# Performance work log

Measured on AMD Instinct MI355X. Metric: run time of the kernel, lower is better.

The kernel has to match this reference:

```python
import jax, jax.numpy as jnp
import numpy as np

THR = 0.2          # config['thr']
BORDER_RM = 2      # config['border_rm']
TEMP = 0.1         # config['dsmax_temperature']


def setup_inputs() -> dict:
    key = jax.random.key(0)
    k0, k1 = jax.random.split(key)
    N, C = 2, 256
    h0c, w0c, h1c, w1c = 60, 80, 60, 80
    return {
        "feat_c0": jax.random.normal(k0, (N, h0c * w0c, C), dtype=jnp.float32),
        "feat_c1": jax.random.normal(k1, (N, h1c * w1c, C), dtype=jnp.float32),
        "h0c": h0c, "w0c": w0c, "h1c": h1c, "w1c": w1c,
    }


def _valid_1d(n: int, b: int):
    # True in the interior [b, n-b), False on the border — matches mask_border writes
    return jnp.zeros((n,), dtype=bool).at[b:n - b].set(True)


def reference(feat_c0, feat_c1, h0c, w0c, h1c, w1c):
    N, L, C = feat_c0.shape
    S = feat_c1.shape[1]
    scale = 1.0 / (C ** 0.5)
    f0 = feat_c0 * scale
    f1 = feat_c1 * scale

    # similarity + dual softmax  -> conf_matrix [N, L, S]
    sim = jnp.einsum('nlc,nsc->nls', f0, f1) / TEMP
    conf = jax.nn.softmax(sim, axis=1) * jax.nn.softmax(sim, axis=2)

    # threshold + border removal (mask_border, vectorized as an interior mask)
    mask = conf > THR
    b = BORDER_RM
    border = (_valid_1d(h0c, b)[:, None, None, None]
              & _valid_1d(w0c, b)[None, :, None, None]
              & _valid_1d(h1c, b)[None, None, :, None]
              & _valid_1d(w1c, b)[None, None, None, :])  # [h0c,w0c,h1c,w1c]
    mask = (mask.reshape(N, h0c, w0c, h1c, w1c) & border[None]).reshape(N, L, S)

    # mutual nearest neighbor
    mask = mask \
        & (conf == conf.max(axis=2, keepdims=True)) \
        & (conf == conf.max(axis=1, keepdims=True))

    # match extraction, expressed densely (static shapes for jit):
    # mask_v[b,i] = row i of pair b has a match; j_ids its column; mconf its confidence
    mask_v = mask.any(axis=2)                               # [N, L]
    j_ids = jnp.argmax(mask, axis=2)                        # [N, L] (first True)
    mconf = jnp.take_along_axis(conf, j_ids[:, :, None], axis=2)[..., 0]
    mconf = jnp.where(mask_v, mconf, 0.0)                   # [N, L]

    # coarse keypoint coords for matched columns: (x, y) = (j % w1c, j // w1c)
    mkpts1_c = jnp.stack([j_ids % w1c, j_ids // w1c], axis=-1)  # [N, L, 2]

    return conf, mask_v, j_ids, mkpts1_c, mconf
```

## Files before the change

### kernel.cpp

```cpp
#include <hip/hip_runtime.h>

typedef _Float16 half8 __attribute__((ext_vector_type(8)));
typedef float f32x4 __attribute__((ext_vector_type(4)));

#define NB 2
#define LS 4800
#define CCH 256
#define W0 80
#define W1 80
#define THRV 0.2f
#define SQS 0.19764235376052370f

#define TN 38
#define PADL 4864

#define OF_RM   0
#define OF_RSI  9600
#define OF_CM   19200
#define OF_CSI  28800
#define OF_RWM  38400
#define OF_CAND 48000
#define OF_CLM  57600
#define OF_PROW 67200
#define OF_PCOL (67200 + 739328)
#define OF_AH   (67200 + 2*739328)
#define OF_BH   (OF_AH + 1228800)

#define O_MASKV 46080000ull
#define O_JIDS  46089600ull
#define O_MKPT  46099200ull
#define O_MCONF 46118400ull

__device__ __forceinline__ void load_lds16(const void* g, void* l) {
    __builtin_amdgcn_global_load_lds((const __attribute__((address_space(1))) void*)g,
                                     (__attribute__((address_space(3))) void*)l, 16, 0, 0);
}

__global__ __launch_bounds__(256) void conv_half(const float* __restrict__ A,
                                                 const float* __restrict__ B,
                                                 float* __restrict__ ws) {
    const int which = blockIdx.y;
    const float* src = which ? B : A;
    _Float16* dst = (_Float16*)(ws + (which ? OF_BH : OF_AH));
    const int idx = blockIdx.x * 256 + threadIdx.x;
    const float4 v = ((const float4*)src)[idx];
    union { _Float16 h[4]; uint2 u; } p;
    p.h[0] = (_Float16)(v.x * SQS);
    p.h[1] = (_Float16)(v.y * SQS);
    p.h[2] = (_Float16)(v.z * SQS);
    p.h[3] = (_Float16)(v.w * SQS);
    ((uint2*)dst)[idx] = p.u;
}

__global__ __launch_bounds__(256, 2) void gemm_mfma(float* __restrict__ out,
                                                    float* __restrict__ ws) {
    __shared__ __align__(16) union {
        struct { _Float16 A[8192]; _Float16 B[8192]; } st;
        struct { float rs[128][2][2]; float cs[128][2][2]; } red;
    } sm;
    const int bx = blockIdx.x, by = blockIdx.y, n = blockIdx.z;
    const _Float16* Ah = (const _Float16*)(ws + OF_AH) + (size_t)n * LS * CCH;
    const _Float16* Bh = (const _Float16*)(ws + OF_BH) + (size_t)n * LS * CCH;
    const int tid = threadIdx.x;
    const int lane = tid & 63, w = tid >> 6;
    const int wx = w & 1, wy = w >> 1;
    const int m = lane & 15, quad = lane >> 4;

    f32x4 acc[4][4];
    {
        f32x4 z = {0.f, 0.f, 0.f, 0.f};
#pragma unroll
        for (int a = 0; a < 4; a++)
#pragma unroll
            for (int b = 0; b < 4; b++) acc[a][b] = z;
    }

    const int srow = lane >> 3;
    const int qst = (lane & 7) ^ (srow & 7);

    for (int kt = 0; kt < 4; kt++) {
        const int k0 = kt * 64;
#pragma unroll
        for (int i = 0; i < 4; i++) {
            const int c = i * 4 + w;
            int gr = by * 128 + c * 8 + srow; gr = gr < LS ? gr : LS - 1;
            load_lds16(Ah + (size_t)gr * CCH + k0 + qst * 8, &sm.st.A[c * 512]);
        }
#pragma unroll
        for (int i = 0; i < 4; i++) {
            const int c = i * 4 + w;
            int gr = bx * 128 + c * 8 + srow; gr = gr < LS ? gr : LS - 1;
            load_lds16(Bh + (size_t)gr * CCH + k0 + qst * 8, &sm.st.B[c * 512]);
        }
        __syncthreads();
#pragma unroll
        for (int t = 0; t < 2; t++) {
            half8 Af[4], Bf[4];
#pragma unroll
            for (int a = 0; a < 4; a++) {
                const int rl = wy * 64 + a * 16 + m;
                const int sl = rl * 8 + ((t * 4 + quad) ^ (rl & 7));
                Af[a] = *(const half8*)&sm.st.A[sl * 8];
            }
#pragma unroll
            for (int b = 0; b < 4; b++) {
                const int cl = wx * 64 + b * 16 + m;
                const int sl = cl * 8 + ((t * 4 + quad) ^ (cl & 7));
                Bf[b] = *(const half8*)&sm.st.B[sl * 8];
            }
#pragma unroll
            for (int a = 0; a < 4; a++)
#pragma unroll
                for (int b = 0; b < 4; b++)
                    acc[a][b] = __builtin_amdgcn_mfma_f32_16x16x32_f16(Af[a], Bf[b], acc[a][b], 0, 0, 0);
        }
        __syncthreads();
    }

    const int l0 = by * 128, s0 = bx * 128;
    float* On = out + (size_t)n * LS * LS;
#pragma unroll
    for (int a = 0; a < 4; a++) {
        const int gr0 = l0 + wy * 64 + a * 16 + quad * 4;
#pragma unroll
        for (int reg = 0; reg < 4; reg++) {
            const int gr = gr0 + reg;
            if (gr < LS) {
#pragma unroll
                for (int b = 0; b < 4; b++) {
                    const int gc = s0 + wx * 64 + b * 16 + m;
                    if (gc < LS) On[(size_t)gr * LS + gc] = acc[a][b][reg];
                }
            }
        }
    }

    bool bval[4];
#pragma unroll
    for (int b = 0; b < 4; b++) bval[b] = (s0 + wx * 64 + b * 16 + m) < LS;
    bool aval[4][4];
#pragma unroll
    for (int a = 0; a < 4; a++)
#pragma unroll
        for (int reg = 0; reg < 4; reg++)
            aval[a][reg] = (l0 + wy * 64 + a * 16 + quad * 4 + reg) < LS;

#pragma unroll
    for (int a = 0; a < 4; a++) {
#pragma unroll
        for (int reg = 0; reg < 4; reg++) {
            float mx = -1e30f;
#pragma unroll
            for (int b = 0; b < 4; b++) if (bval[b]) mx = fmaxf(mx, acc[a][b][reg]);
            for (int d = 1; d < 16; d <<= 1) mx = fmaxf(mx, __shfl_xor(mx, d, 64));
            float sum = 0.f;
#pragma unroll
            for (int b = 0; b < 4; b++) if (bval[b]) sum += __expf(acc[a][b][reg] - mx);
            for (int d = 1; d < 16; d <<= 1) sum += __shfl_xor(sum, d, 64);
            if (m == 0) {
                const int rl = wy * 64 + a * 16 + quad * 4 + reg;
                sm.red.rs[rl][wx][0] = mx; sm.red.rs[rl][wx][1] = sum;
            }
        }
    }
#pragma unroll
    for (int b = 0; b < 4; b++) {
        float mx = -1e30f;
#pragma unroll
        for (int a = 0; a < 4; a++)
#pragma unroll
            for (int reg = 0; reg < 4; reg++)
                if (aval[a][reg]) mx = fmaxf(mx, acc[a][b][reg]);
        float sum = 0.f;
#pragma unroll
        for (int a = 0; a < 4; a++)
#pragma unroll
            for (int reg = 0; reg < 4; reg++)
                if (aval[a][reg]) sum += __expf(acc[a][b][reg] - mx);
        for (int d = 16; d < 64; d <<= 1) {
            const float mo = __shfl_xor(mx, d, 64);
            const float so = __shfl_xor(sum, d, 64);
            const float nm = fmaxf(mx, mo);
            sum = sum * __expf(mx - nm) + so * __expf(mo - nm);
            mx = nm;
        }
        if (quad == 0) {
            const int cl = wx * 64 + b * 16 + m;
            sm.red.cs[cl][wy][0] = mx; sm.red.cs[cl][wy][1] = sum;
        }
    }
    __syncthreads();
    if (tid < 128) {
        const float m0 = sm.red.rs[tid][0][0], v0 = sm.red.rs[tid][0][1];
        const float m1 = sm.red.rs[tid][1][0], v1 = sm.red.rs[tid][1][1];
        const float nm = fmaxf(m0, m1);
        const float s = v0 * __expf(m0 - nm) + v1 * __expf(m1 - nm);
        ((float2*)(ws + OF_PROW))[((size_t)n * TN + bx) * PADL + by * 128 + tid] = make_float2(nm, s);
    } else {
        const int t = tid - 128;
        const float m0 = sm.red.cs[t][0][0], v0 = sm.red.cs[t][0][1];
        const float m1 = sm.red.cs[t][1][0], v1 = sm.red.cs[t][1][1];
        const float nm = fmaxf(m0, m1);
        const float s = v0 * __expf(m0 - nm) + v1 * __expf(m1 - nm);
        ((float2*)(ws + OF_PCOL))[((size_t)n * TN + by) * PADL + bx * 128 + t] = make_float2(nm, s);
    }
}

__global__ __launch_bounds__(256) void combine_stats(float* __restrict__ ws) {
    const int idx = blockIdx.x * 256 + threadIdx.x;
    const int half_ = idx >= 9600;
    const int i = idx - half_ * 9600;
    const int n = i / LS, r = i % LS;
    const float2* P = (const float2*)(ws + (half_ ? OF_PCOL : OF_PROW)) + (size_t)n * TN * PADL + r;
    float M = -1e30f, S = 0.f;
    for (int b = 0; b < TN; b++) {
        const float2 p = P[(size_t)b * PADL];
        const float nm = fmaxf(M, p.x);
        S = S * __expf(M - nm) + p.y * __expf(p.x - nm);
        M = nm;
    }
    if (!half_) {
        ws[OF_RM + i] = M; ws[OF_RSI + i] = 1.0f / S;
        ws[OF_CLM + i] = 0.0f;
    } else {
        ws[OF_CM + i] = M; ws[OF_CSI + i] = 1.0f / S;
    }
}

__global__ __launch_bounds__(256) void conf_pass(float* __restrict__ conf,
                                                 float* __restrict__ ws) {
    const int chunk = blockIdx.x, n = blockIdx.y;
    const int tid = threadIdx.x;
    const int r0 = chunk * 16;
    __shared__ float Lv[16][256];
    __shared__ int Li[16][256];
    __shared__ float Mv[16][16];
    __shared__ int Mi[16][16];
    float cmv[19], csiv[19], cmax[19];
#pragma unroll
    for (int j = 0; j < 19; j++) {
        const int s = tid + j * 256;
        cmax[j] = 0.f;
        if (s < LS) { cmv[j] = ws[OF_CM + n * LS + s]; csiv[j] = ws[OF_CSI + n * LS + s]; }
        else { cmv[j] = 0.f; csiv[j] = 0.f; }
    }
    for (int r = 0; r < 16; r++) {
        const int gr = r0 + r;
        const float rm = ws[OF_RM + n * LS + gr];
        const float rsi = ws[OF_RSI + n * LS + gr];
        float* row = conf + ((size_t)n * LS + gr) * LS;
        float lmax = -1.f; int lidx = 0;
#pragma unroll
        for (int j = 0; j < 19; j++) {
            const int s = tid + j * 256;
            if (s < LS) {
                const float x = row[s];
                const float c = __expf(2.f * x - rm - cmv[j]) * (rsi * csiv[j]);
                row[s] = c;
                cmax[j] = fmaxf(cmax[j], c);
                if (c > lmax) { lmax = c; lidx = s; }
            }
        }
        Lv[r][tid] = lmax; Li[r][tid] = lidx;
    }
    __syncthreads();
    {
        const int r = tid >> 4, p = tid & 15;
        float bv = -2.f; int bi = 0;
        for (int k = 0; k < 16; k++) {
            const float v = Lv[r][p * 16 + k]; const int ii = Li[r][p * 16 + k];
            if (v > bv || (v == bv && ii < bi)) { bv = v; bi = ii; }
        }
        Mv[r][p] = bv; Mi[r][p] = bi;
    }
    __syncthreads();
    if (tid < 16) {
        float bv = -2.f; int bi = 0;
        for (int p = 0; p < 16; p++) {
            const float v = Mv[tid][p]; const int ii = Mi[tid][p];
            if (v > bv || (v == bv && ii < bi)) { bv = v; bi = ii; }
        }
        ws[OF_RWM + n * LS + r0 + tid] = bv;
        ((int*)ws)[OF_CAND + n * LS + r0 + tid] = bi;
    }
    int* clm = (int*)ws + OF_CLM + n * LS;
#pragma unroll
    for (int j = 0; j < 19; j++) {
        const int s = tid + j * 256;
        if (s < LS && cmax[j] > 0.f) atomicMax(&clm[s], __float_as_int(cmax[j]));
    }
}

__global__ __launch_bounds__(256) void match_pass(const float* __restrict__ ws,
                                                  float* __restrict__ out) {
    const int idx = blockIdx.x * 256 + threadIdx.x;
    if (idx >= NB * LS) return;
    const int n = idx / LS, l = idx % LS;
    const float rwm = ws[OF_RWM + idx];
    const int cand = ((const int*)ws)[OF_CAND + idx];
    const float clm = ws[OF_CLM + n * LS + cand];
    const int y0 = l / W0, x0 = l % W0;
    const int y1 = cand / W1, x1 = cand % W1;
    const bool b0 = (y0 >= 2 && y0 < 58 && x0 >= 2 && x0 < 78);
    const bool b1 = (y1 >= 2 && y1 < 58 && x1 >= 2 && x1 < 78);
    const bool matched = (rwm > THRV) && b0 && b1 && (rwm == clm);
    const int j = matched ? cand : 0;
    out[O_MASKV + idx] = matched ? 1.f : 0.f;
    out[O_JIDS + idx] = (float)j;
    out[O_MKPT + (size_t)idx * 2 + 0] = (float)(j % W1);
    out[O_MKPT + (size_t)idx * 2 + 1] = (float)(j / W1);
    out[O_MCONF + idx] = matched ? rwm : 0.f;
}

extern "C" void kernel_launch(void* const* d_in, const int* in_sizes, int n_in,
                              void* d_out, int out_size, void* d_ws, size_t ws_size,
                              hipStream_t stream) {
    const float* f0 = (const float*)d_in[0];
    const float* f1 = (const float*)d_in[1];
    float* out = (float*)d_out;
    float* ws = (float*)d_ws;

    conv_half<<<dim3(2400, 2), 256, 0, stream>>>(f0, f1, ws);
    gemm_mfma<<<dim3(TN, TN, NB), 256, 0, stream>>>(out, ws);
    combine_stats<<<75, 256, 0, stream>>>(ws);
    conf_pass<<<dim3(300, NB), 256, 0, stream>>>(out, ws);
    match_pass<<<38, 256, 0, stream>>>(ws, out);
}
```

Measured before the change: 326.1 us.

## Recompute GEMM to fuse dual-softmax epilogue and avoid storing raw similarity

```diff
diff --git a/kernel.cpp b/kernel.cpp
--- a/kernel.cpp
+++ b/kernel.cpp
@@ -22,8 +22,10 @@
 #define OF_CAND 48000
 #define OF_CLM  57600
 #define OF_PROW 67200
-#define OF_PCOL (67200 + 739328)
-#define OF_AH   (67200 + 2*739328)
+#define OF_PCOL (OF_PROW + 739328)
+#define OF_PRWM (OF_PCOL + 739328)
+#define OF_PCLM (OF_PRWM + 739328)
+#define OF_AH   (OF_PCLM + 369664)
 #define OF_BH   (OF_AH + 1228800)
 
 #define O_MASKV 46080000ull
@@ -52,8 +54,58 @@
     ((uint2*)dst)[idx] = p.u;
 }
 
-__global__ __launch_bounds__(256, 2) void gemm_mfma(float* __restrict__ out,
-                                                    float* __restrict__ ws) {
+#define GEMM_KLOOP(SMEM)                                                        \
+    const int lane = tid & 63, w = tid >> 6;                                    \
+    const int wx = w & 1, wy = w >> 1;                                          \
+    const int m = lane & 15, quad = lane >> 4;                                  \
+    f32x4 acc[4][4];                                                            \
+    {                                                                           \
+        f32x4 z = {0.f, 0.f, 0.f, 0.f};                                        \
+        for (int a = 0; a < 4; a++)                                             \
+            for (int b = 0; b < 4; b++) acc[a][b] = z;                          \
+    }                                                                           \
+    const int srow = lane >> 3;                                                 \
+    const int qst = (lane & 7) ^ (srow & 7);                                    \
+    for (int kt = 0; kt < 4; kt++) {                                            \
+        const int k0 = kt * 64;                                                 \
+        _Pragma("unroll")                                                       \
+        for (int i = 0; i < 4; i++) {                                           \
+            const int c = i * 4 + w;                                            \
+            int gr = by * 128 + c * 8 + srow; gr = gr < LS ? gr : LS - 1;       \
+            load_lds16(Ah + (size_t)gr * CCH + k0 + qst * 8, &SMEM.st.A[c * 512]); \
+        }                                                                       \
+        _Pragma("unroll")                                                       \
+        for (int i = 0; i < 4; i++) {                                           \
+            const int c = i * 4 + w;                                            \
+            int gr = bx * 128 + c * 8 + srow; gr = gr < LS ? gr : LS - 1;       \
+            load_lds16(Bh + (size_t)gr * CCH + k0 + qst * 8, &SMEM.st.B[c * 512]); \
+        }                                                                       \
+        __syncthreads();                                                        \
+        _Pragma("unroll")                                                       \
+        for (int t = 0; t < 2; t++) {                                           \
+            half8 Af[4], Bf[4];                                                 \
+            _Pragma("unroll")                                                   \
+            for (int a = 0; a < 4; a++) {                                       \
+                const int rl = wy * 64 + a * 16 + m;                            \
+                const int sl = rl * 8 + ((t * 4 + quad) ^ (rl & 7));            \
+                Af[a] = *(const half8*)&SMEM.st.A[sl * 8];                      \
+            }                                                                   \
+            _Pragma("unroll")                                                   \
+            for (int b = 0; b < 4; b++) {                                       \
+                const int cl = wx * 64 + b * 16 + m;                            \
+                const int sl = cl * 8 + ((t * 4 + quad) ^ (cl & 7));            \
+                Bf[b] = *(const half8*)&SMEM.st.B[sl * 8];                      \
+            }                                                                   \
+            _Pragma("unroll")                                                   \
+            for (int a = 0; a < 4; a++)                                         \
+                _Pragma("unroll")                                               \
+                for (int b = 0; b < 4; b++)                                     \
+                    acc[a][b] = __builtin_amdgcn_mfma_f32_16x16x32_f16(Af[a], Bf[b], acc[a][b], 0, 0, 0); \
+        }                                                                       \
+        __syncthreads();                                                        \
+    }
+
+__global__ __launch_bounds__(256, 2) void gemm_stats(float* __restrict__ ws) {
     __shared__ __align__(16) union {
         struct { _Float16 A[8192]; _Float16 B[8192]; } st;
         struct { float rs[128][2][2]; float cs[128][2][2]; } red;
@@ -62,79 +114,10 @@
     const _Float16* Ah = (const _Float16*)(ws + OF_AH) + (size_t)n * LS * CCH;
     const _Float16* Bh = (const _Float16*)(ws + OF_BH) + (size_t)n * LS * CCH;
     const int tid = threadIdx.x;
-    const int lane = tid & 63, w = tid >> 6;
-    const int wx = w & 1, wy = w >> 1;
-    const int m = lane & 15, quad = lane >> 4;
-
-    f32x4 acc[4][4];
-    {
-        f32x4 z = {0.f, 0.f, 0.f, 0.f};
-#pragma unroll
-        for (int a = 0; a < 4; a++)
-#pragma unroll
-            for (int b = 0; b < 4; b++) acc[a][b] = z;
-    }
-
-    const int srow = lane >> 3;
-    const int qst = (lane & 7) ^ (srow & 7);
-
-    for (int kt = 0; kt < 4; kt++) {
-        const int k0 = kt * 64;
-#pragma unroll
-        for (int i = 0; i < 4; i++) {
-            const int c = i * 4 + w;
-            int gr = by * 128 + c * 8 + srow; gr = gr < LS ? gr : LS - 1;
-            load_lds16(Ah + (size_t)gr * CCH + k0 + qst * 8, &sm.st.A[c * 512]);
-        }
-#pragma unroll
-        for (int i = 0; i < 4; i++) {
-            const int c = i * 4 + w;
-            int gr = bx * 128 + c * 8 + srow; gr = gr < LS ? gr : LS - 1;
-            load_lds16(Bh + (size_t)gr * CCH + k0 + qst * 8, &sm.st.B[c * 512]);
-        }
-        __syncthreads();
-#pragma unroll
-        for (int t = 0; t < 2; t++) {
-            half8 Af[4], Bf[4];
-#pragma unroll
-            for (int a = 0; a < 4; a++) {
-                const int rl = wy * 64 + a * 16 + m;
-                const int sl = rl * 8 + ((t * 4 + quad) ^ (rl & 7));
-                Af[a] = *(const half8*)&sm.st.A[sl * 8];
-            }
-#pragma unroll
-            for (int b = 0; b < 4; b++) {
-                const int cl = wx * 64 + b * 16 + m;
-                const int sl = cl * 8 + ((t * 4 + quad) ^ (cl & 7));
-                Bf[b] = *(const half8*)&sm.st.B[sl * 8];
-            }
-#pragma unroll
-            for (int a = 0; a < 4; a++)
-#pragma unroll
-                for (int b = 0; b < 4; b++)
-                    acc[a][b] = __builtin_amdgcn_mfma_f32_16x16x32_f16(Af[a], Bf[b], acc[a][b], 0, 0, 0);
-        }
-        __syncthreads();
-    }
+
+    GEMM_KLOOP(sm)
 
     const int l0 = by * 128, s0 = bx * 128;
-    float* On = out + (size_t)n * LS * LS;
-#pragma unroll
-    for (int a = 0; a < 4; a++) {
-        const int gr0 = l0 + wy * 64 + a * 16 + quad * 4;
-#pragma unroll
-        for (int reg = 0; reg < 4; reg++) {
-            const int gr = gr0 + reg;
-            if (gr < LS) {
-#pragma unroll
-                for (int b = 0; b < 4; b++) {
-                    const int gc = s0 + wx * 64 + b * 16 + m;
-                    if (gc < LS) On[(size_t)gr * LS + gc] = acc[a][b][reg];
-                }
-            }
-        }
-    }
-
     bool bval[4];
 #pragma unroll
     for (int b = 0; b < 4; b++) bval[b] = (s0 + wx * 64 + b * 16 + m) < LS;
@@ -208,6 +191,7 @@
 
 __global__ __launch_bounds__(256) void combine_stats(float* __restrict__ ws) {
     const int idx = blockIdx.x * 256 + threadIdx.x;
+    if (idx >= 2 * NB * LS) return;
     const int half_ = idx >= 9600;
     const int i = idx - half_ * 9600;
     const int n = i / LS, r = i % LS;
@@ -219,75 +203,149 @@
         S = S * __expf(M - nm) + p.y * __expf(p.x - nm);
         M = nm;
     }
+    if (!half_) { ws[OF_RM + i] = M; ws[OF_RSI + i] = 1.0f / S; }
+    else        { ws[OF_CM + i] = M; ws[OF_CSI + i] = 1.0f / S; }
+}
+
+__global__ __launch_bounds__(256, 2) void gemm_conf(float* __restrict__ out,
+                                                    float* __restrict__ ws) {
+    __shared__ __align__(16) union {
+        struct { _Float16 A[8192]; _Float16 B[8192]; } st;
+        struct {
+            float rowst[128][2];
+            float colst[128][2];
+            float rv[128][2][2];
+            float cv[128][2];
+        } ep;
+    } sm;
+    const int bx = blockIdx.x, by = blockIdx.y, n = blockIdx.z;
+    const _Float16* Ah = (const _Float16*)(ws + OF_AH) + (size_t)n * LS * CCH;
+    const _Float16* Bh = (const _Float16*)(ws + OF_BH) + (size_t)n * LS * CCH;
+    const int tid = threadIdx.x;
+
+    GEMM_KLOOP(sm)
+
+    const int l0 = by * 128, s0 = bx * 128;
+    if (tid < 128) {
+        int gr = l0 + tid; gr = gr < LS ? gr : LS - 1;
+        sm.ep.rowst[tid][0] = ws[OF_RM + n * LS + gr];
+        sm.ep.rowst[tid][1] = ws[OF_RSI + n * LS + gr];
+    } else {
+        const int lc = tid - 128;
+        int gc = s0 + lc; gc = gc < LS ? gc : LS - 1;
+        sm.ep.colst[lc][0] = ws[OF_CM + n * LS + gc];
+        sm.ep.colst[lc][1] = ws[OF_CSI + n * LS + gc];
+    }
+    __syncthreads();
+
+    float* On = out + (size_t)n * LS * LS;
+    bool bval[4]; int gcol[4];
+#pragma unroll
+    for (int b = 0; b < 4; b++) {
+        gcol[b] = s0 + wx * 64 + b * 16 + m;
+        bval[b] = gcol[b] < LS;
+    }
+#pragma unroll
+    for (int a = 0; a < 4; a++) {
+        const int lr0 = wy * 64 + a * 16 + quad * 4;
+#pragma unroll
+        for (int reg = 0; reg < 4; reg++) {
+            const int lr = lr0 + reg;
+            const float rm = sm.ep.rowst[lr][0], rsi = sm.ep.rowst[lr][1];
+            const bool rok = (l0 + lr) < LS;
+#pragma unroll
+            for (int b = 0; b < 4; b++) {
+                const int lc = wx * 64 + b * 16 + m;
+                const float cmv = sm.ep.colst[lc][0], csi = sm.ep.colst[lc][1];
+                const float x = acc[a][b][reg];
+                const float c = __expf(2.f * x - rm - cmv) * (rsi * csi);
+                acc[a][b][reg] = c;
+                if (rok && bval[b]) On[(size_t)(l0 + lr) * LS + gcol[b]] = c;
+            }
+        }
+    }
+
+#pragma unroll
+    for (int a = 0; a < 4; a++) {
+#pragma unroll
+        for (int reg = 0; reg < 4; reg++) {
+            float v = -1.f; int ii = 0;
+#pragma unroll
+            for (int b = 0; b < 4; b++) {
+                if (bval[b]) {
+                    const float c = acc[a][b][reg];
+                    if (c > v) { v = c; ii = gcol[b]; }
+                }
+            }
+            for (int d = 1; d < 16; d <<= 1) {
+                const float vo = __shfl_xor(v, d, 64);
+                const int io = __shfl_xor(ii, d, 64);
+                if (vo > v || (vo == v && io < ii)) { v = vo; ii = io; }
+            }
+            if (m == 0) {
+                const int rl = wy * 64 + a * 16 + quad * 4 + reg;
+                sm.ep.rv[rl][wx][0] = v;
+                sm.ep.rv[rl][wx][1] = __int_as_float(ii);
+            }
+        }
+    }
+    bool aval[4][4];
+#pragma unroll
+    for (int a = 0; a < 4; a++)
+#pragma unroll
+        for (int reg = 0; reg < 4; reg++)
+            aval[a][reg] = (l0 + wy * 64 + a * 16 + quad * 4 + reg) < LS;
+#pragma unroll
+    for (int b = 0; b < 4; b++) {
+        float v = -1.f;
+#pragma unroll
+        for (int a = 0; a < 4; a++)
+#pragma unroll
+            for (int reg = 0; reg < 4; reg++)
+                if (aval[a][reg]) v = fmaxf(v, acc[a][b][reg]);
+        for (int d = 16; d < 64; d <<= 1) v = fmaxf(v, __shfl_xor(v, d, 64));
+        if (quad == 0) {
+            const int cl = wx * 64 + b * 16 + m;
+            sm.ep.cv[cl][wy] = v;
+        }
+    }
+    __syncthreads();
+    if (tid < 128) {
+        const float v0 = sm.ep.rv[tid][0][0], v1 = sm.ep.rv[tid][1][0];
+        const int i0 = __float_as_int(sm.ep.rv[tid][0][1]);
+        const int i1 = __float_as_int(sm.ep.rv[tid][1][1]);
+        float v; int ii;
+        if (v1 > v0 || (v1 == v0 && i1 < i0)) { v = v1; ii = i1; } else { v = v0; ii = i0; }
+        ((float2*)(ws + OF_PRWM))[((size_t)n * TN + bx) * PADL + by * 128 + tid] =
+            make_float2(v, __int_as_float(ii));
+    } else {
+        const int t = tid - 128;
+        (ws + OF_PCLM)[((size_t)n * TN + by) * PADL + bx * 128 + t] =
+            fmaxf(sm.ep.cv[t][0], sm.ep.cv[t][1]);
+    }
+}
+
+__global__ __launch_bounds__(256) void combine2(float* __restrict__ ws) {
+    const int idx = blockIdx.x * 256 + threadIdx.x;
+    if (idx >= 2 * NB * LS) return;
+    const int half_ = idx >= 9600;
+    const int i = idx - half_ * 9600;
+    const int n = i / LS, r = i % LS;
     if (!half_) {
-        ws[OF_RM + i] = M; ws[OF_RSI + i] = 1.0f / S;
-        ws[OF_CLM + i] = 0.0f;
+        const float2* P = (const float2*)(ws + OF_PRWM) + (size_t)n * TN * PADL + r;
+        float v = -1.f; int ii = 0;
+        for (int b = 0; b < TN; b++) {
+            const float2 p = P[(size_t)b * PADL];
+            const int pi = __float_as_int(p.y);
+            if (p.x > v || (p.x == v && pi < ii)) { v = p.x; ii = pi; }
+        }
+        ws[OF_RWM + i] = v;
+        ((int*)ws)[OF_CAND + i] = ii;
     } else {
-        ws[OF_CM + i] = M; ws[OF_CSI + i] = 1.0f / S;
-    }
-}
-
-__global__ __launch_bounds__(256) void conf_pass(float* __restrict__ conf,
-                                                 float* __restrict__ ws) {
-    const int chunk = blockIdx.x, n = blockIdx.y;
-    const int tid = threadIdx.x;
-    const int r0 = chunk * 16;
-    __shared__ float Lv[16][256];
-    __shared__ int Li[16][256];
-    __shared__ float Mv[16][16];
-    __shared__ int Mi[16][16];
-    float cmv[19], csiv[19], cmax[19];
-#pragma unroll
-    for (int j = 0; j < 19; j++) {
-        const int s = tid + j * 256;
-        cmax[j] = 0.f;
-        if (s < LS) { cmv[j] = ws[OF_CM + n * LS + s]; csiv[j] = ws[OF_CSI + n * LS + s]; }
-        else { cmv[j] = 0.f; csiv[j] = 0.f; }
-    }
-    for (int r = 0; r < 16; r++) {
-        const int gr = r0 + r;
-        const float rm = ws[OF_RM + n * LS + gr];
-        const float rsi = ws[OF_RSI + n * LS + gr];
-        float* row = conf + ((size_t)n * LS + gr) * LS;
-        float lmax = -1.f; int lidx = 0;
-#pragma unroll
-        for (int j = 0; j < 19; j++) {
-            const int s = tid + j * 256;
-            if (s < LS) {
-                const float x = row[s];
-                const float c = __expf(2.f * x - rm - cmv[j]) * (rsi * csiv[j]);
-                row[s] = c;
-                cmax[j] = fmaxf(cmax[j], c);
-                if (c > lmax) { lmax = c; lidx = s; }
-            }
-        }
-        Lv[r][tid] = lmax; Li[r][tid] = lidx;
-    }
-    __syncthreads();
-    {
-        const int r = tid >> 4, p = tid & 15;
-        float bv = -2.f; int bi = 0;
-        for (int k = 0; k < 16; k++) {
-            const float v = Lv[r][p * 16 + k]; const int ii = Li[r][p * 16 + k];
-            if (v > bv || (v == bv && ii < bi)) { bv = v; bi = ii; }
-        }
-        Mv[r][p] = bv; Mi[r][p] = bi;
-    }
-    __syncthreads();
-    if (tid < 16) {
-        float bv = -2.f; int bi = 0;
-        for (int p = 0; p < 16; p++) {
-            const float v = Mv[tid][p]; const int ii = Mi[tid][p];
-            if (v > bv || (v == bv && ii < bi)) { bv = v; bi = ii; }
-        }
-        ws[OF_RWM + n * LS + r0 + tid] = bv;
-        ((int*)ws)[OF_CAND + n * LS + r0 + tid] = bi;
-    }
-    int* clm = (int*)ws + OF_CLM + n * LS;
-#pragma unroll
-    for (int j = 0; j < 19; j++) {
-        const int s = tid + j * 256;
-        if (s < LS && cmax[j] > 0.f) atomicMax(&clm[s], __float_as_int(cmax[j]));
+        const float* P = ws + OF_PCLM + (size_t)n * TN * PADL + r;
+        float v = -1.f;
+        for (int b = 0; b < TN; b++) v = fmaxf(v, P[(size_t)b * PADL]);
+        ws[OF_CLM + i] = v;
     }
 }
 
@@ -321,8 +379,9 @@
     float* ws = (float*)d_ws;
 
     conv_half<<<dim3(2400, 2), 256, 0, stream>>>(f0, f1, ws);
-    gemm_mfma<<<dim3(TN, TN, NB), 256, 0, stream>>>(out, ws);
+    gemm_stats<<<dim3(TN, TN, NB), 256, 0, stream>>>(ws);
     combine_stats<<<75, 256, 0, stream>>>(ws);
-    conf_pass<<<dim3(300, NB), 256, 0, stream>>>(out, ws);
+    gemm_conf<<<dim3(TN, TN, NB), 256, 0, stream>>>(out, ws);
+    combine2<<<75, 256, 0, stream>>>(ws);
     match_pass<<<38, 256, 0, stream>>>(ws, out);
 }
```

After: 337.2 us. +3.4%, slower.
